# Kernel tuning notes

Hardware: AMD Instinct MI355X
Metric: run time of the kernel (lower is better)

## Reference

```python
import jax, jax.numpy as jnp
import numpy as np

BATCH, SEQ, IN, HID, LAYERS, OUT = 32, 1024, 1024, 1024, 4, 1024


def setup_inputs() -> dict:
    key = jax.random.key(0)
    ks = jax.random.split(key, 6)
    s_in = 1.0 / np.sqrt(IN)
    s_h = 1.0 / np.sqrt(HID)
    x = jax.random.normal(ks[0], (BATCH, SEQ, IN), dtype=jnp.float32)
    # stacked per-layer params (input_size == hidden_size so shapes are uniform)
    Wi = jax.random.normal(ks[1], (LAYERS, IN, HID), dtype=jnp.float32) * s_in
    Wh = jax.random.normal(ks[2], (LAYERS, HID, HID), dtype=jnp.float32) * s_h
    b = jnp.zeros((LAYERS, HID), dtype=jnp.float32)
    fcW = jax.random.normal(ks[3], (HID, OUT), dtype=jnp.float32) * s_h
    fcb = jnp.zeros((OUT,), dtype=jnp.float32)
    return {"x": x, "Wi": Wi, "Wh": Wh, "b": b, "fcW": fcW, "fcb": fcb}


def reference(x, Wi, Wh, b, fcW, fcb):
    # Stacked Elman RNN: h_t = tanh(x_t @ Wi + b + h_{t-1} @ Wh), per layer.
    seq = x  # [B, T, H]
    num_layers = Wi.shape[0]
    for l in range(num_layers):
        wi, wh, bl = Wi[l], Wh[l], b[l]
        # precompute input projection for the whole sequence (one big GEMM)
        xp = jnp.einsum('bti,ih->bth', seq, wi) + bl  # [B, T, H]

        def step(h, xt):
            h_new = jnp.tanh(xt + h @ wh)
            return h_new, h_new

        h0 = jnp.zeros((seq.shape[0], wh.shape[0]), dtype=seq.dtype)
        _, ys = jax.lax.scan(step, h0, jnp.swapaxes(xp, 0, 1))  # [T, B, H]
        seq = jnp.swapaxes(ys, 0, 1)
    # last timestep of final layer -> dense head
    return seq[:, -1, :] @ fcW + fcb
```

## Files before the change

### kernel.cpp

```cpp
#include <hip/hip_runtime.h>
#include <hip/hip_fp16.h>

#define B_   32
#define T_   1024
#define H_   1024
#define NL_  4
#define NBLK 256
#define NTHR 256

typedef _Float16 half8  __attribute__((ext_vector_type(8)));
typedef _Float16 half2t __attribute__((ext_vector_type(2)));
typedef float    f32x4  __attribute__((ext_vector_type(4)));

__device__ __forceinline__ unsigned long long a_load_u64(const void* p) {
  return __hip_atomic_load((unsigned long long*)p, __ATOMIC_RELAXED,
                           __HIP_MEMORY_SCOPE_AGENT);
}
__device__ __forceinline__ half8 a_load_h8(const _Float16* p) {
  struct Q { unsigned long long a, b; } s;
  s.a = a_load_u64(p);
  s.b = a_load_u64(p + 4);
  return __builtin_bit_cast(half8, s);
}
__device__ __forceinline__ void a_store_u32(void* p, unsigned v) {
  __hip_atomic_store((unsigned*)p, v, __ATOMIC_RELAXED,
                     __HIP_MEMORY_SCOPE_AGENT);
}

__device__ __forceinline__ void gbar(unsigned* flags, unsigned ep) {
  __syncthreads();
  if (threadIdx.x == 0)
    __hip_atomic_store(&flags[blockIdx.x], ep, __ATOMIC_RELAXED,
                       __HIP_MEMORY_SCOPE_AGENT);
  if (threadIdx.x < 64) {
    const int ln = threadIdx.x;
    for (;;) {
      unsigned f0 = __hip_atomic_load(&flags[ln],       __ATOMIC_RELAXED, __HIP_MEMORY_SCOPE_AGENT);
      unsigned f1 = __hip_atomic_load(&flags[64 + ln],  __ATOMIC_RELAXED, __HIP_MEMORY_SCOPE_AGENT);
      unsigned f2 = __hip_atomic_load(&flags[128 + ln], __ATOMIC_RELAXED, __HIP_MEMORY_SCOPE_AGENT);
      unsigned f3 = __hip_atomic_load(&flags[192 + ln], __ATOMIC_RELAXED, __HIP_MEMORY_SCOPE_AGENT);
      if (__all(f0 >= ep && f1 >= ep && f2 >= ep && f3 >= ep)) break;
      __builtin_amdgcn_s_sleep(1);
    }
  }
  __syncthreads();
  asm volatile("" ::: "memory");
}

__device__ __forceinline__ half8 cvt8(const float* p) {
  float4 u = *(const float4*)p;
  float4 v = *(const float4*)(p + 4);
  half8 r;
  r[0]=(_Float16)u.x; r[1]=(_Float16)u.y; r[2]=(_Float16)u.z; r[3]=(_Float16)u.w;
  r[4]=(_Float16)v.x; r[5]=(_Float16)v.y; r[6]=(_Float16)v.z; r[7]=(_Float16)v.w;
  return r;
}

extern "C" __global__ void __launch_bounds__(NTHR)
rnn_persist(const float* __restrict__ x,  const float* __restrict__ Wi,
            const float* __restrict__ Wh, const float* __restrict__ bias,
            const float* __restrict__ fcW,const float* __restrict__ fcb,
            float* __restrict__ out, unsigned char* __restrict__ ws)
{
  __shared__ float red[8*256];
  __shared__ float blds[16];

  unsigned* flags = (unsigned*)ws;
  _Float16* hbuf  = (_Float16*)(ws + 65536);
  float*    hlast = (float*)(ws + 65536 + (size_t)NL_*2*B_*H_*2);

  const int tid = threadIdx.x;
  const int bid = blockIdx.x;
  const int l   = bid >> 6;
  const int cb  = bid & 63;
  const int wv  = tid >> 6;
  const int ln  = tid & 63;
  const int lq  = ln & 15;
  const int lg  = ln >> 4;

  half8 bfr[16];
  {
    const float* Wl  = Wi + (size_t)l*H_*H_;
    const float* Whl = Wh + (size_t)l*H_*H_;
    #pragma unroll
    for (int q = 0; q < 8; ++q) {
      const int kt = wv*8 + q;
      const float* s0 = Wl  + (size_t)(kt*32 + lg*8)*H_ + cb*16 + lq;
      const float* s1 = Whl + (size_t)(kt*32 + lg*8)*H_ + cb*16 + lq;
      half8 f0, f1;
      #pragma unroll
      for (int j = 0; j < 8; ++j) {
        f0[j] = (_Float16)s0[(size_t)j*H_];
        f1[j] = (_Float16)s1[(size_t)j*H_];
      }
      bfr[q]   = f0;
      bfr[8+q] = f1;
    }
  }
  if (tid < 16) blds[tid] = bias[l*H_ + cb*16 + tid];

  unsigned ep = 0;

  for (int s = 0; s < T_ + NL_ - 1; ++s) {
    const int t = s - l;
    if ((unsigned)t < (unsigned)T_) {
      f32x4 acc0 = {0.f,0.f,0.f,0.f};
      f32x4 acc1 = {0.f,0.f,0.f,0.f};

      if (l == 0) {
        const float* px = x + (size_t)lq*(T_*H_) + (size_t)t*H_ + lg*8;
        #pragma unroll
        for (int q = 0; q < 8; ++q) {
          const int kt = wv*8 + q;
          half8 a0 = cvt8(px + kt*32);
          half8 a1 = cvt8(px + (size_t)16*(T_*H_) + kt*32);
          acc0 = __builtin_amdgcn_mfma_f32_16x16x32_f16(a0, bfr[q], acc0, 0,0,0);
          acc1 = __builtin_amdgcn_mfma_f32_16x16x32_f16(a1, bfr[q], acc1, 0,0,0);
        }
      } else {
        const _Float16* pi = hbuf + ((l-1)*2 + (t&1))*(B_*H_) + lq*H_ + lg*8;
        #pragma unroll
        for (int q = 0; q < 8; ++q) {
          const int kt = wv*8 + q;
          half8 a0 = a_load_h8(pi + kt*32);
          half8 a1 = a_load_h8(pi + 16*H_ + kt*32);
          acc0 = __builtin_amdgcn_mfma_f32_16x16x32_f16(a0, bfr[q], acc0, 0,0,0);
          acc1 = __builtin_amdgcn_mfma_f32_16x16x32_f16(a1, bfr[q], acc1, 0,0,0);
        }
      }
      if (t > 0) {
        const _Float16* ph = hbuf + (l*2 + ((t-1)&1))*(B_*H_) + lq*H_ + lg*8;
        #pragma unroll
        for (int q = 0; q < 8; ++q) {
          const int kt = wv*8 + q;
          half8 a0 = a_load_h8(ph + kt*32);
          half8 a1 = a_load_h8(ph + 16*H_ + kt*32);
          acc0 = __builtin_amdgcn_mfma_f32_16x16x32_f16(a0, bfr[8+q], acc0, 0,0,0);
          acc1 = __builtin_amdgcn_mfma_f32_16x16x32_f16(a1, bfr[8+q], acc1, 0,0,0);
        }
      }

      *(f32x4*)(red + (wv*2+0)*256 + lq*16 + lg*4) = acc0;
      *(f32x4*)(red + (wv*2+1)*256 + lq*16 + lg*4) = acc1;
      __syncthreads();

      const int r   = tid >> 3;
      const int cp  = tid & 7;
      const int c0  = cp*2, c1 = c0 + 1;
      const int m   = r >> 4;
      const int r15 = r & 15;
      const float* p0 = red + m*256 + r15;
      float s0 = p0[c0*16] + p0[c0*16+512] + p0[c0*16+1024] + p0[c0*16+1536];
      float s1 = p0[c1*16] + p0[c1*16+512] + p0[c1*16+1024] + p0[c1*16+1536];
      const float h0 = tanhf(s0 + blds[c0]);
      const float h1 = tanhf(s1 + blds[c1]);
      half2t v2 = { (_Float16)h0, (_Float16)h1 };
      _Float16* ho = hbuf + (l*2 + (t&1))*(B_*H_) + (size_t)r*H_ + cb*16 + c0;
      a_store_u32(ho, __builtin_bit_cast(unsigned, v2));
      if (l == NL_-1 && t == T_-1) {
        a_store_u32(&hlast[(size_t)r*H_ + cb*16 + c0], __builtin_bit_cast(unsigned, h0));
        a_store_u32(&hlast[(size_t)r*H_ + cb*16 + c1], __builtin_bit_cast(unsigned, h1));
      }
    }
    ++ep;
    gbar(flags, ep);
  }

  if (tid < 128) {
    const int c = bid*4 + (tid & 3);
    const int b = tid >> 2;
    const float* hv = hlast + (size_t)b*H_;
    const float* wp = fcW + c;
    float a0 = 0.f, a1 = 0.f;
    for (int k = 0; k < H_; k += 2) {
      float2 f = __builtin_bit_cast(float2, a_load_u64(hv + k));
      a0 += f.x * wp[(size_t)k*H_];
      a1 += f.y * wp[(size_t)(k+1)*H_];
    }
    out[(size_t)b*H_ + c] = fcb[c] + a0 + a1;
  }
}

extern "C" void kernel_launch(void* const* d_in, const int* in_sizes, int n_in,
                              void* d_out, int out_size, void* d_ws, size_t ws_size,
                              hipStream_t stream) {
  const float* x   = (const float*)d_in[0];
  const float* Wi  = (const float*)d_in[1];
  const float* Wh  = (const float*)d_in[2];
  const float* b   = (const float*)d_in[3];
  const float* fcW = (const float*)d_in[4];
  const float* fcb = (const float*)d_in[5];
  float* out = (float*)d_out;
  unsigned char* ws = (unsigned char*)d_ws;

  hipMemsetAsync(d_ws, 0, 65536, stream);

  void* args[] = { (void*)&x, (void*)&Wi, (void*)&Wh, (void*)&b,
                   (void*)&fcW, (void*)&fcb, (void*)&out, (void*)&ws };
  hipLaunchCooperativeKernel((const void*)rnn_persist, dim3(NBLK), dim3(NTHR),
                             args, 0, stream);
}
```

Baseline: 18.44 ms.

## Replace global barrier with per-layer dataflow flags and 4-deep hidden ring buffer

Drops the grid-wide barrier that ran after every wavefront step. Each layer's 64 blocks now wait only on their own layer's previous-step flags and on the lower layer's current-step flags, with back-pressure from the upper layer through a 4-deep ring of hidden-state buffers. The input-projection MFMAs are issued before waiting on the same-layer recurrence flag, which overlaps that work with synchronization. The goal is to cut barrier latency and let layers drift relative to each other; it adds more flag polling and relies on relaxed atomics being visible in the right order.

```diff
diff --git a/kernel.cpp b/kernel.cpp
--- a/kernel.cpp
+++ b/kernel.cpp
@@ -1,19 +1,23 @@
 #include <hip/hip_runtime.h>
 #include <hip/hip_fp16.h>
 
-#define B_   32
-#define T_   1024
-#define H_   1024
-#define NL_  4
-#define NBLK 256
-#define NTHR 256
+#define B_    32
+#define T_    1024
+#define H_    1024
+#define NL_   4
+#define NBLK  256
+#define NTHR  256
+#define DEPTH 4
 
 typedef _Float16 half8  __attribute__((ext_vector_type(8)));
 typedef _Float16 half2t __attribute__((ext_vector_type(2)));
 typedef float    f32x4  __attribute__((ext_vector_type(4)));
 
+__device__ __forceinline__ unsigned a_load_u32(const unsigned* p) {
+  return __hip_atomic_load(p, __ATOMIC_RELAXED, __HIP_MEMORY_SCOPE_AGENT);
+}
 __device__ __forceinline__ unsigned long long a_load_u64(const void* p) {
-  return __hip_atomic_load((unsigned long long*)p, __ATOMIC_RELAXED,
+  return __hip_atomic_load((const unsigned long long*)p, __ATOMIC_RELAXED,
                            __HIP_MEMORY_SCOPE_AGENT);
 }
 __device__ __forceinline__ half8 a_load_h8(const _Float16* p) {
@@ -25,26 +29,6 @@
 __device__ __forceinline__ void a_store_u32(void* p, unsigned v) {
   __hip_atomic_store((unsigned*)p, v, __ATOMIC_RELAXED,
                      __HIP_MEMORY_SCOPE_AGENT);
-}
-
-__device__ __forceinline__ void gbar(unsigned* flags, unsigned ep) {
-  __syncthreads();
-  if (threadIdx.x == 0)
-    __hip_atomic_store(&flags[blockIdx.x], ep, __ATOMIC_RELAXED,
-                       __HIP_MEMORY_SCOPE_AGENT);
-  if (threadIdx.x < 64) {
-    const int ln = threadIdx.x;
-    for (;;) {
-      unsigned f0 = __hip_atomic_load(&flags[ln],       __ATOMIC_RELAXED, __HIP_MEMORY_SCOPE_AGENT);
-      unsigned f1 = __hip_atomic_load(&flags[64 + ln],  __ATOMIC_RELAXED, __HIP_MEMORY_SCOPE_AGENT);
-      unsigned f2 = __hip_atomic_load(&flags[128 + ln], __ATOMIC_RELAXED, __HIP_MEMORY_SCOPE_AGENT);
-      unsigned f3 = __hip_atomic_load(&flags[192 + ln], __ATOMIC_RELAXED, __HIP_MEMORY_SCOPE_AGENT);
-      if (__all(f0 >= ep && f1 >= ep && f2 >= ep && f3 >= ep)) break;
-      __builtin_amdgcn_s_sleep(1);
-    }
-  }
-  __syncthreads();
-  asm volatile("" ::: "memory");
 }
 
 __device__ __forceinline__ half8 cvt8(const float* p) {
@@ -67,7 +51,7 @@
 
   unsigned* flags = (unsigned*)ws;
   _Float16* hbuf  = (_Float16*)(ws + 65536);
-  float*    hlast = (float*)(ws + 65536 + (size_t)NL_*2*B_*H_*2);
+  float*    hlast = (float*)(ws + 65536 + (size_t)NL_*DEPTH*B_*H_*2);
 
   const int tid = threadIdx.x;
   const int bid = blockIdx.x;
@@ -99,72 +83,104 @@
   }
   if (tid < 16) blds[tid] = bias[l*H_ + cb*16 + tid];
 
-  unsigned ep = 0;
-
-  for (int s = 0; s < T_ + NL_ - 1; ++s) {
-    const int t = s - l;
-    if ((unsigned)t < (unsigned)T_) {
-      f32x4 acc0 = {0.f,0.f,0.f,0.f};
-      f32x4 acc1 = {0.f,0.f,0.f,0.f};
-
-      if (l == 0) {
-        const float* px = x + (size_t)lq*(T_*H_) + (size_t)t*H_ + lg*8;
-        #pragma unroll
-        for (int q = 0; q < 8; ++q) {
-          const int kt = wv*8 + q;
-          half8 a0 = cvt8(px + kt*32);
-          half8 a1 = cvt8(px + (size_t)16*(T_*H_) + kt*32);
-          acc0 = __builtin_amdgcn_mfma_f32_16x16x32_f16(a0, bfr[q], acc0, 0,0,0);
-          acc1 = __builtin_amdgcn_mfma_f32_16x16x32_f16(a1, bfr[q], acc1, 0,0,0);
-        }
-      } else {
-        const _Float16* pi = hbuf + ((l-1)*2 + (t&1))*(B_*H_) + lq*H_ + lg*8;
-        #pragma unroll
-        for (int q = 0; q < 8; ++q) {
-          const int kt = wv*8 + q;
-          half8 a0 = a_load_h8(pi + kt*32);
-          half8 a1 = a_load_h8(pi + 16*H_ + kt*32);
-          acc0 = __builtin_amdgcn_mfma_f32_16x16x32_f16(a0, bfr[q], acc0, 0,0,0);
-          acc1 = __builtin_amdgcn_mfma_f32_16x16x32_f16(a1, bfr[q], acc1, 0,0,0);
-        }
-      }
-      if (t > 0) {
-        const _Float16* ph = hbuf + (l*2 + ((t-1)&1))*(B_*H_) + lq*H_ + lg*8;
-        #pragma unroll
-        for (int q = 0; q < 8; ++q) {
-          const int kt = wv*8 + q;
-          half8 a0 = a_load_h8(ph + kt*32);
-          half8 a1 = a_load_h8(ph + 16*H_ + kt*32);
-          acc0 = __builtin_amdgcn_mfma_f32_16x16x32_f16(a0, bfr[8+q], acc0, 0,0,0);
-          acc1 = __builtin_amdgcn_mfma_f32_16x16x32_f16(a1, bfr[8+q], acc1, 0,0,0);
-        }
-      }
-
-      *(f32x4*)(red + (wv*2+0)*256 + lq*16 + lg*4) = acc0;
-      *(f32x4*)(red + (wv*2+1)*256 + lq*16 + lg*4) = acc1;
-      __syncthreads();
-
-      const int r   = tid >> 3;
-      const int cp  = tid & 7;
-      const int c0  = cp*2, c1 = c0 + 1;
-      const int m   = r >> 4;
-      const int r15 = r & 15;
-      const float* p0 = red + m*256 + r15;
-      float s0 = p0[c0*16] + p0[c0*16+512] + p0[c0*16+1024] + p0[c0*16+1536];
-      float s1 = p0[c1*16] + p0[c1*16+512] + p0[c1*16+1024] + p0[c1*16+1536];
-      const float h0 = tanhf(s0 + blds[c0]);
-      const float h1 = tanhf(s1 + blds[c1]);
-      half2t v2 = { (_Float16)h0, (_Float16)h1 };
-      _Float16* ho = hbuf + (l*2 + (t&1))*(B_*H_) + (size_t)r*H_ + cb*16 + c0;
-      a_store_u32(ho, __builtin_bit_cast(unsigned, v2));
-      if (l == NL_-1 && t == T_-1) {
-        a_store_u32(&hlast[(size_t)r*H_ + cb*16 + c0], __builtin_bit_cast(unsigned, h0));
-        a_store_u32(&hlast[(size_t)r*H_ + cb*16 + c1], __builtin_bit_cast(unsigned, h1));
-      }
-    }
-    ++ep;
-    gbar(flags, ep);
-  }
+  for (int t = 0; t < T_; ++t) {
+    if (tid < 64) {
+      for (;;) {
+        bool ok = true;
+        if (l > 0)
+          ok &= (int)a_load_u32(&flags[(l-1)*64 + ln]) >= t + 1;
+        if (l < NL_-1)
+          ok &= (int)a_load_u32(&flags[(l+1)*64 + ln]) >= t - (DEPTH-1);
+        if (__all(ok)) break;
+        __builtin_amdgcn_s_sleep(1);
+      }
+    }
+    __syncthreads();
+    asm volatile("" ::: "memory");
+
+    f32x4 acc0 = {0.f,0.f,0.f,0.f};
+    f32x4 acc1 = {0.f,0.f,0.f,0.f};
+
+    if (l == 0) {
+      const float* px = x + (size_t)lq*(T_*H_) + (size_t)t*H_ + lg*8;
+      #pragma unroll
+      for (int q = 0; q < 8; ++q) {
+        const int kt = wv*8 + q;
+        half8 a0 = cvt8(px + kt*32);
+        half8 a1 = cvt8(px + (size_t)16*(T_*H_) + kt*32);
+        acc0 = __builtin_amdgcn_mfma_f32_16x16x32_f16(a0, bfr[q], acc0, 0,0,0);
+        acc1 = __builtin_amdgcn_mfma_f32_16x16x32_f16(a1, bfr[q], acc1, 0,0,0);
+      }
+    } else {
+      const _Float16* pi = hbuf + ((size_t)((l-1)*DEPTH + (t&3)))*(B_*H_) + lq*H_ + lg*8;
+      #pragma unroll
+      for (int q = 0; q < 8; ++q) {
+        const int kt = wv*8 + q;
+        half8 a0 = a_load_h8(pi + kt*32);
+        half8 a1 = a_load_h8(pi + 16*H_ + kt*32);
+        acc0 = __builtin_amdgcn_mfma_f32_16x16x32_f16(a0, bfr[q], acc0, 0,0,0);
+        acc1 = __builtin_amdgcn_mfma_f32_16x16x32_f16(a1, bfr[q], acc1, 0,0,0);
+      }
+    }
+
+    if (tid < 64) {
+      for (;;) {
+        bool ok = (int)a_load_u32(&flags[l*64 + ln]) >= t;
+        if (__all(ok)) break;
+        __builtin_amdgcn_s_sleep(1);
+      }
+    }
+    __syncthreads();
+    asm volatile("" ::: "memory");
+
+    if (t > 0) {
+      const _Float16* ph = hbuf + ((size_t)(l*DEPTH + ((t-1)&3)))*(B_*H_) + lq*H_ + lg*8;
+      #pragma unroll
+      for (int q = 0; q < 8; ++q) {
+        const int kt = wv*8 + q;
+        half8 a0 = a_load_h8(ph + kt*32);
+        half8 a1 = a_load_h8(ph + 16*H_ + kt*32);
+        acc0 = __builtin_amdgcn_mfma_f32_16x16x32_f16(a0, bfr[8+q], acc0, 0,0,0);
+        acc1 = __builtin_amdgcn_mfma_f32_16x16x32_f16(a1, bfr[8+q], acc1, 0,0,0);
+      }
+    }
+
+    *(f32x4*)(red + (wv*2+0)*256 + lq*16 + lg*4) = acc0;
+    *(f32x4*)(red + (wv*2+1)*256 + lq*16 + lg*4) = acc1;
+    __syncthreads();
+
+    const int r   = tid >> 3;
+    const int cp  = tid & 7;
+    const int c0  = cp*2, c1 = c0 + 1;
+    const int m   = r >> 4;
+    const int r15 = r & 15;
+    const float* p0 = red + m*256 + r15;
+    float s0 = p0[c0*16] + p0[c0*16+512] + p0[c0*16+1024] + p0[c0*16+1536];
+    float s1 = p0[c1*16] + p0[c1*16+512] + p0[c1*16+1024] + p0[c1*16+1536];
+    const float h0 = tanhf(s0 + blds[c0]);
+    const float h1 = tanhf(s1 + blds[c1]);
+    half2t v2 = { (_Float16)h0, (_Float16)h1 };
+    _Float16* ho = hbuf + ((size_t)(l*DEPTH + (t&3)))*(B_*H_) + (size_t)r*H_ + cb*16 + c0;
+    a_store_u32(ho, __builtin_bit_cast(unsigned, v2));
+    if (l == NL_-1 && t == T_-1) {
+      a_store_u32(&hlast[(size_t)r*H_ + cb*16 + c0], __builtin_bit_cast(unsigned, h0));
+      a_store_u32(&hlast[(size_t)r*H_ + cb*16 + c1], __builtin_bit_cast(unsigned, h1));
+    }
+
+    __syncthreads();
+    if (tid == 0)
+      a_store_u32(&flags[l*64 + cb], (unsigned)(t + 1));
+  }
+
+  if (tid < 64) {
+    for (;;) {
+      bool ok = (int)a_load_u32(&flags[(NL_-1)*64 + ln]) >= T_;
+      if (__all(ok)) break;
+      __builtin_amdgcn_s_sleep(1);
+    }
+  }
+  __syncthreads();
+  asm volatile("" ::: "memory");
 
   if (tid < 128) {
     const int c = bid*4 + (tid & 3);
```

Result: faster. 15.05 ms (-18.4%).
